# Optimization experiments

Hardware: AMD Instinct MI355X
Metric: run time of the kernel (lower is better)

The kernel has to match this reference:

```python
import jax, jax.numpy as jnp
import numpy as np

B, S, D, H = 4, 1024, 1024, 16
HD = D // H
EPS = 1e-5


def _layernorm(x, g, b):
    m = jnp.mean(x, axis=-1, keepdims=True)
    v = jnp.mean((x - m) ** 2, axis=-1, keepdims=True)
    return (x - m) * jax.lax.rsqrt(v + EPS) * g + b


def setup_inputs() -> dict:
    key = jax.random.key(0)
    ks = jax.random.split(key, 8)
    sc = 1.0 / np.sqrt(D)
    return {
        "x": jax.random.normal(ks[0], (B, S, D), dtype=jnp.float32),
        "seq_len": jax.random.randint(ks[1], (B,), 1, S + 1, dtype=jnp.int32),
        "Wq": jax.random.normal(ks[2], (D, D), dtype=jnp.float32) * sc,
        "bq": jnp.zeros((D,), dtype=jnp.float32),
        "Wk": jax.random.normal(ks[3], (D, D), dtype=jnp.float32) * sc,
        "bk": jnp.zeros((D,), dtype=jnp.float32),
        "Wv": jax.random.normal(ks[4], (D, D), dtype=jnp.float32) * sc,
        "bv": jnp.zeros((D,), dtype=jnp.float32),
        "ln_g": jnp.ones((HD,), dtype=jnp.float32),
        "ln_b": jnp.zeros((HD,), dtype=jnp.float32),
    }


def reference(x, seq_len, Wq, bq, Wk, bk, Wv, bv, ln_g, ln_b):
    # Faithful quirk: k and v are projections of the ALREADY projected q.
    q = x @ Wq.T + bq                      # [B,S,D]
    k = q @ Wk.T + bk
    v = q @ Wv.T + bv
    # [B,S,D] -> [B,H,S,HD]
    def split_heads(t):
        return t.reshape(B, S, H, HD).transpose(0, 2, 1, 3)
    q, k, v = split_heads(q), split_heads(k), split_heads(v)
    # shared per-head LayerNorm over head_dim
    q = _layernorm(q, ln_g, ln_b)
    k = _layernorm(k, ln_g, ln_b)
    v = _layernorm(v, ln_g, ln_b)
    # raw scores (no temperature scaling in the original; temperature=1.0 unused)
    scores = jnp.einsum("bhqd,bhkd->bhqk", q, k)
    # encoder_mask: multiplicative validity mask on key positions, repeated per head
    mask = (jnp.arange(S)[None, :] < seq_len[:, None]).astype(scores.dtype)  # [B,S]
    scores = scores * mask[:, None, None, :]
    attn = jax.nn.softmax(scores, axis=-1)
    # dropout is identity at inference
    out = jnp.einsum("bhqk,bhkd->bhqd", attn, v)
    return out.transpose(0, 2, 1, 3).reshape(B, S, D)
```

## Files before the change

### kernel.cpp

```cpp
#include <hip/hip_runtime.h>

#define B_  4
#define S_  1024
#define D_  1024
#define H_  16
#define HD_ 64
#define EPS_ 1e-5f

typedef _Float16 f16x8 __attribute__((ext_vector_type(8)));
typedef _Float16 f16x4 __attribute__((ext_vector_type(4)));
typedef __bf16 bf16x8 __attribute__((ext_vector_type(8)));
typedef float  f32x4  __attribute__((ext_vector_type(4)));
typedef unsigned short ushort8v __attribute__((ext_vector_type(8)));

static __device__ __forceinline__ unsigned short f2bf(float f) {
  union { float f; unsigned u; } v; v.f = f;
  unsigned r = v.u + 0x7fffu + ((v.u >> 16) & 1u);
  return (unsigned short)(r >> 16);
}
static __device__ __forceinline__ float bf2f(unsigned short u) {
  union { unsigned u; float f; } v; v.u = ((unsigned)u) << 16;
  return v.f;
}

#define GLD16(gp, lp) __builtin_amdgcn_global_load_lds( \
    (const __attribute__((address_space(1))) void*)(gp), \
    (__attribute__((address_space(3))) void*)(lp), 16, 0, 0)

__global__ __launch_bounds__(256) void cvt_all(
    const float* __restrict__ x,  _Float16* __restrict__ xh,
    const float* __restrict__ Wq, _Float16* __restrict__ wqh,
    const float* __restrict__ Wk, _Float16* __restrict__ wkh,
    const float* __restrict__ Wv, _Float16* __restrict__ wvh,
    float* __restrict__ Vtail) {
  int bid = blockIdx.x;
  if (bid >= 7168) {
    int i = (bid - 7168) * 1024 + threadIdx.x * 4;
    *(float4*)(Vtail + i) = make_float4(0.f, 0.f, 0.f, 0.f);
    return;
  }
  const float* src; _Float16* dst; int base;
  if (bid < 4096)      { src = x;  dst = xh;  base = bid; }
  else if (bid < 5120) { src = Wq; dst = wqh; base = bid - 4096; }
  else if (bid < 6144) { src = Wk; dst = wkh; base = bid - 5120; }
  else                 { src = Wv; dst = wvh; base = bid - 6144; }
  int i = base * 1024 + threadIdx.x * 4;
  float4 f = *(const float4*)(src + i);
  f16x4 h;
  h.x = (_Float16)f.x; h.y = (_Float16)f.y; h.z = (_Float16)f.z; h.w = (_Float16)f.w;
  *(f16x4*)(dst + i) = h;
}

__global__ __launch_bounds__(256, 2) void gemm_bt_bias(
    const _Float16* __restrict__ A,
    const _Float16* __restrict__ B0, const float* __restrict__ bias0,
    _Float16* __restrict__ C0,
    const _Float16* __restrict__ B1, const float* __restrict__ bias1,
    _Float16* __restrict__ C1,
    int M, int N, int K)
{
  const _Float16* Bm = blockIdx.z ? B1 : B0;
  const float* bias  = blockIdx.z ? bias1 : bias0;
  _Float16* C        = blockIdx.z ? C1 : C0;

  __shared__ _Float16 As[2 * 128 * 32];
  __shared__ _Float16 Bs[2 * 64 * 32];

  int tid  = threadIdx.x;
  int lane = tid & 63;
  int wave = tid >> 6;
  int wm = wave >> 1, wn = wave & 1;
  int qd = lane >> 4, l15 = lane & 15;

  long row0 = (long)blockIdx.y * 128;
  long col0 = (long)blockIdx.x * 64;

  int r_a = tid >> 2;
  int c_a = (tid & 3) * 8;

  f32x4 acc[4][2] = {};

  for (int kk = 0; kk < K; kk += 64) {
    GLD16(A  + (row0 + r_a) * K + kk + c_a,           As + tid * 8);
    GLD16(A  + (row0 + 64 + r_a) * K + kk + c_a,      As + 2048 + tid * 8);
    GLD16(A  + (row0 + r_a) * K + kk + 32 + c_a,      As + 4096 + tid * 8);
    GLD16(A  + (row0 + 64 + r_a) * K + kk + 32 + c_a, As + 6144 + tid * 8);
    GLD16(Bm + (col0 + r_a) * K + kk + c_a,           Bs + tid * 8);
    GLD16(Bm + (col0 + r_a) * K + kk + 32 + c_a,      Bs + 2048 + tid * 8);
    __syncthreads();

    for (int ks = 0; ks < 2; ks++) {
      f16x8 af[4], bfr[2];
      for (int t = 0; t < 4; t++)
        af[t]  = *(const f16x8*)(As + ks * 4096 + (wm * 64 + t * 16 + l15) * 32 + qd * 8);
      for (int j = 0; j < 2; j++)
        bfr[j] = *(const f16x8*)(Bs + ks * 2048 + (wn * 32 + j * 16 + l15) * 32 + qd * 8);
      for (int i = 0; i < 4; i++)
        for (int j = 0; j < 2; j++)
          acc[i][j] = __builtin_amdgcn_mfma_f32_16x16x32_f16(af[i], bfr[j], acc[i][j], 0, 0, 0);
    }
    __syncthreads();
  }

  for (int i = 0; i < 4; i++) {
    long row = row0 + wm * 64 + i * 16 + qd * 4;
    for (int j = 0; j < 2; j++) {
      long col = col0 + wn * 32 + j * 16 + l15;
      float bv = bias[col];
      for (int r = 0; r < 4; r++)
        C[(row + r) * N + col] = (_Float16)(acc[i][j][r] + bv);
    }
  }
}

__global__ __launch_bounds__(256, 2) void gemm_bt_bias128(
    const _Float16* __restrict__ A,
    const _Float16* __restrict__ B0, const float* __restrict__ bias0,
    _Float16* __restrict__ C0,
    const _Float16* __restrict__ B1, const float* __restrict__ bias1,
    _Float16* __restrict__ C1,
    int M, int N, int K)
{
  const _Float16* Bm = blockIdx.z ? B1 : B0;
  const float* bias  = blockIdx.z ? bias1 : bias0;
  _Float16* C        = blockIdx.z ? C1 : C0;

  __shared__ _Float16 As[2 * 128 * 32];
  __shared__ _Float16 Bs[2 * 128 * 32];

  int tid  = threadIdx.x;
  int lane = tid & 63;
  int wave = tid >> 6;
  int wm = wave >> 1, wn = wave & 1;
  int qd = lane >> 4, l15 = lane & 15;

  long row0 = (long)blockIdx.y * 128;
  long col0 = (long)blockIdx.x * 128;

  int r_a = tid >> 2;
  int c_a = (tid & 3) * 8;

  f32x4 acc[4][4] = {};

  for (int kk = 0; kk < K; kk += 64) {
    GLD16(A  + (row0 + r_a) * K + kk + c_a,           As + tid * 8);
    GLD16(A  + (row0 + 64 + r_a) * K + kk + c_a,      As + 2048 + tid * 8);
    GLD16(A  + (row0 + r_a) * K + kk + 32 + c_a,      As + 4096 + tid * 8);
    GLD16(A  + (row0 + 64 + r_a) * K + kk + 32 + c_a, As + 6144 + tid * 8);
    GLD16(Bm + (col0 + r_a) * K + kk + c_a,           Bs + tid * 8);
    GLD16(Bm + (col0 + 64 + r_a) * K + kk + c_a,      Bs + 2048 + tid * 8);
    GLD16(Bm + (col0 + r_a) * K + kk + 32 + c_a,      Bs + 4096 + tid * 8);
    GLD16(Bm + (col0 + 64 + r_a) * K + kk + 32 + c_a, Bs + 6144 + tid * 8);
    __syncthreads();

    for (int ks = 0; ks < 2; ks++) {
      f16x8 af[4], bfr[4];
      for (int t = 0; t < 4; t++) {
        af[t]  = *(const f16x8*)(As + ks * 4096 + (wm * 64 + t * 16 + l15) * 32 + qd * 8);
        bfr[t] = *(const f16x8*)(Bs + ks * 4096 + (wn * 64 + t * 16 + l15) * 32 + qd * 8);
      }
      for (int i = 0; i < 4; i++)
        for (int j = 0; j < 4; j++)
          acc[i][j] = __builtin_amdgcn_mfma_f32_16x16x32_f16(af[i], bfr[j], acc[i][j], 0, 0, 0);
    }
    __syncthreads();
  }

  for (int i = 0; i < 4; i++) {
    long row = row0 + wm * 64 + i * 16 + qd * 4;
    for (int j = 0; j < 4; j++) {
      long col = col0 + wn * 64 + j * 16 + l15;
      float bv = bias[col];
      for (int r = 0; r < 4; r++)
        C[(row + r) * N + col] = (_Float16)(acc[i][j][r] + bv);
    }
  }
}

__global__ __launch_bounds__(256) void ln_qkv(
    const _Float16* __restrict__ qh,
    const _Float16* __restrict__ kh,
    const _Float16* __restrict__ vh,
    const float* __restrict__ ln_g, const float* __restrict__ ln_b,
    const int* __restrict__ seq_len,
    _Float16* __restrict__ Qn,
    _Float16* __restrict__ Kn,
    unsigned short* __restrict__ Vt,
    float* __restrict__ Vtail)
{
  __shared__ unsigned short Vls[256][68];
  int tid = threadIdx.x;
  int s0 = blockIdx.x * 256;
  int h = blockIdx.y, b = blockIdx.z;
  long bh = (long)b * H_ + h;
  long s = s0 + tid;
  long inbase  = ((long)b * S_ + s) * D_ + (long)h * HD_;
  long outbase = (bh * S_ + s) * HD_;

  f16x8 rq[8], rk[8], rv[8];
  for (int i = 0; i < 8; i++) {
    rq[i] = *(const f16x8*)(qh + inbase + i * 8);
    rk[i] = *(const f16x8*)(kh + inbase + i * 8);
    rv[i] = *(const f16x8*)(vh + inbase + i * 8);
  }

  {
    float sum = 0.f, sq = 0.f;
    for (int i = 0; i < 8; i++)
      for (int j = 0; j < 8; j++) { float xv = (float)rq[i][j]; sum += xv; sq = fmaf(xv, xv, sq); }
    float m = sum * (1.f / 64.f);
    float inv = rsqrtf(sq * (1.f / 64.f) - m * m + EPS_);
    for (int i = 0; i < 8; i++) {
      f16x8 o;
      for (int j = 0; j < 8; j++)
        o[j] = (_Float16)(((float)rq[i][j] - m) * inv * ln_g[i * 8 + j] + ln_b[i * 8 + j]);
      *(f16x8*)(Qn + outbase + i * 8) = o;
    }
  }
  {
    float sum = 0.f, sq = 0.f;
    for (int i = 0; i < 8; i++)
      for (int j = 0; j < 8; j++) { float xv = (float)rk[i][j]; sum += xv; sq = fmaf(xv, xv, sq); }
    float m = sum * (1.f / 64.f);
    float inv = rsqrtf(sq * (1.f / 64.f) - m * m + EPS_);
    for (int i = 0; i < 8; i++) {
      f16x8 o;
      for (int j = 0; j < 8; j++)
        o[j] = (_Float16)(((float)rk[i][j] - m) * inv * ln_g[i * 8 + j] + ln_b[i * 8 + j]);
      *(f16x8*)(Kn + outbase + i * 8) = o;
    }
  }
  {
    float sum = 0.f, sq = 0.f;
    for (int i = 0; i < 8; i++)
      for (int j = 0; j < 8; j++) { float xv = (float)rv[i][j]; sum += xv; sq = fmaf(xv, xv, sq); }
    float m = sum * (1.f / 64.f);
    float inv = rsqrtf(sq * (1.f / 64.f) - m * m + EPS_);
    for (int i = 0; i < 8; i++)
      for (int j = 0; j < 8; j++)
        Vls[tid][i * 8 + j] = f2bf(((float)rv[i][j] - m) * inv * ln_g[i * 8 + j] + ln_b[i * 8 + j]);
  }
  __syncthreads();
  int d = tid >> 2, sc = tid & 3;
  int len = seq_len[b];
  long vbase = (bh * HD_ + d) * S_ + s0 + sc * 64;
  float tsum = 0.f;
  for (int j0 = 0; j0 < 64; j0 += 8) {
    ushort8v w;
    for (int jj = 0; jj < 8; jj++) {
      unsigned short ub = Vls[sc * 64 + j0 + jj][d];
      w[jj] = ub;
      if (s0 + sc * 64 + j0 + jj >= len) tsum += bf2f(ub);
    }
    *(ushort8v*)(Vt + vbase + j0) = w;
  }
  if (s0 + sc * 64 + 64 > len)
    atomicAdd(&Vtail[bh * HD_ + d], tsum);
}

__global__ __launch_bounds__(256, 4) void attn(
    const _Float16* __restrict__ Qn,
    const _Float16* __restrict__ Kn,
    const unsigned short* __restrict__ Vt,
    const float* __restrict__ Vtail,
    const int* __restrict__ seq_len,
    float* __restrict__ out)
{
  __shared__ _Float16 Ks[2][64 * 32];
  __shared__ unsigned short Vts[2][64 * 32];
  __shared__ __bf16 Ps[4][16 * 72];

  int tid = threadIdx.x, lane = tid & 63, wave = tid >> 6;
  int qd = lane >> 4, l15 = lane & 15;
  int b = blockIdx.x;
  int h = blockIdx.y;
  int q0 = blockIdx.z * 64;
  long bh = (long)b * H_ + h;
  int len = seq_len[b];
  int ntile = (len + 63) >> 6;

  int skey = tid >> 2;
  int schunk = (tid & 3) * 8;

  f16x8 qf[2];
  {
    const _Float16* qp = Qn + (bh * S_ + q0 + wave * 16 + l15) * HD_;
    qf[0] = *(const f16x8*)(qp + qd * 8);
    qf[1] = *(const f16x8*)(qp + 32 + qd * 8);
  }
  float tv[4];
  for (int t = 0; t < 4; t++) tv[t] = Vtail[bh * HD_ + t * 16 + l15];

  f32x4 o[4] = {};
  float den[4] = {0.f, 0.f, 0.f, 0.f};

  for (int kt = 0; kt < ntile; kt++) {
    GLD16(Kn + (bh * S_ + kt * 64 + skey) * HD_ + schunk,      &Ks[0][0] + tid * 8);
    GLD16(Kn + (bh * S_ + kt * 64 + skey) * HD_ + 32 + schunk, &Ks[1][0] + tid * 8);
    GLD16(Vt + (bh * HD_ + skey) * S_ + kt * 64 + schunk,      &Vts[0][0] + tid * 8);
    GLD16(Vt + (bh * HD_ + skey) * S_ + kt * 64 + 32 + schunk, &Vts[1][0] + tid * 8);
    __syncthreads();

    f32x4 sacc[4] = {};
    for (int tn = 0; tn < 4; tn++) {
      f16x8 kf0 = *(const f16x8*)(&Ks[0][0] + (tn * 16 + l15) * 32 + qd * 8);
      f16x8 kf1 = *(const f16x8*)(&Ks[1][0] + (tn * 16 + l15) * 32 + qd * 8);
      sacc[tn] = __builtin_amdgcn_mfma_f32_16x16x32_f16(qf[0], kf0, sacc[tn], 0, 0, 0);
      sacc[tn] = __builtin_amdgcn_mfma_f32_16x16x32_f16(qf[1], kf1, sacc[tn], 0, 0, 0);
    }

    if (kt * 64 + 64 <= len) {
      for (int tn = 0; tn < 4; tn++)
        for (int r = 0; r < 4; r++) {
          float p = __expf(sacc[tn][r]);
          __bf16 pb = (__bf16)p;
          den[r] += (float)pb;
          Ps[wave][(qd * 4 + r) * 72 + tn * 16 + l15] = pb;
        }
    } else {
      for (int tn = 0; tn < 4; tn++) {
        int kg = kt * 64 + tn * 16 + l15;
        bool valid = kg < len;
        for (int r = 0; r < 4; r++) {
          float p = valid ? __expf(sacc[tn][r]) : 0.f;
          __bf16 pb = (__bf16)p;
          den[r] += (float)pb;
          Ps[wave][(qd * 4 + r) * 72 + tn * 16 + l15] = pb;
        }
      }
    }

    bf16x8 pf0 = *(const bf16x8*)(&Ps[wave][l15 * 72 + qd * 8]);
    bf16x8 pf1 = *(const bf16x8*)(&Ps[wave][l15 * 72 + 32 + qd * 8]);
    for (int t = 0; t < 4; t++) {
      bf16x8 vf0 = *(const bf16x8*)(&Vts[0][0] + (t * 16 + l15) * 32 + qd * 8);
      bf16x8 vf1 = *(const bf16x8*)(&Vts[1][0] + (t * 16 + l15) * 32 + qd * 8);
      o[t] = __builtin_amdgcn_mfma_f32_16x16x32_bf16(pf0, vf0, o[t], 0, 0, 0);
      o[t] = __builtin_amdgcn_mfma_f32_16x16x32_bf16(pf1, vf1, o[t], 0, 0, 0);
    }
    __syncthreads();
  }

  for (int t = 0; t < 4; t++)
    for (int r = 0; r < 4; r++) o[t][r] += tv[t];

  float tden = (float)(S_ - len);
  for (int r = 0; r < 4; r++) {
    for (int off = 1; off < 16; off <<= 1)
      den[r] += __shfl_xor(den[r], off, 64);
    den[r] += tden;
  }

  for (int t = 0; t < 4; t++)
    for (int r = 0; r < 4; r++) {
      long s = q0 + wave * 16 + qd * 4 + r;
      long dcol = (long)h * HD_ + t * 16 + l15;
      out[((long)b * S_ + s) * D_ + dcol] = o[t][r] / den[r];
    }
}

extern "C" void kernel_launch(void* const* d_in, const int* in_sizes, int n_in,
                              void* d_out, int out_size, void* d_ws, size_t ws_size,
                              hipStream_t stream) {
  const float* x     = (const float*)d_in[0];
  const int*  seq    = (const int*)d_in[1];
  const float* Wq    = (const float*)d_in[2];
  const float* bq    = (const float*)d_in[3];
  const float* Wk    = (const float*)d_in[4];
  const float* bk    = (const float*)d_in[5];
  const float* Wv    = (const float*)d_in[6];
  const float* bv    = (const float*)d_in[7];
  const float* ln_g  = (const float*)d_in[8];
  const float* ln_b  = (const float*)d_in[9];
  float* out = (float*)d_out;

  char* ws = (char*)d_ws;
  _Float16* xh  = (_Float16*)(ws);
  _Float16* wqh = (_Float16*)(ws + (8l  << 20));
  _Float16* wkh = (_Float16*)(ws + (10l << 20));
  _Float16* wvh = (_Float16*)(ws + (12l << 20));
  float*    Vtail = (float*)(ws + (14l << 20));
  _Float16* qh  = (_Float16*)(ws + (16l << 20));
  _Float16* kh  = (_Float16*)(ws + (24l << 20));
  _Float16* vh  = (_Float16*)(ws + (32l << 20));
  _Float16* Qn  = (_Float16*)(ws + (40l << 20));
  _Float16* Kn  = (_Float16*)(ws + (48l << 20));
  unsigned short* Vt = (unsigned short*)(ws + (56l << 20));

  cvt_all<<<7172, 256, 0, stream>>>(x, xh, Wq, wqh, Wk, wkh, Wv, wvh, Vtail);

  dim3 g1(D_ / 64, (B_ * S_) / 128, 1);
  gemm_bt_bias<<<g1, 256, 0, stream>>>(xh, wqh, bq, qh, wqh, bq, qh,
                                       B_ * S_, D_, D_);
  dim3 g2(D_ / 128, (B_ * S_) / 128, 2);
  gemm_bt_bias128<<<g2, 256, 0, stream>>>(qh, wkh, bk, kh, wvh, bv, vh,
                                          B_ * S_, D_, D_);

  dim3 g3(S_ / 256, H_, B_);
  ln_qkv<<<g3, 256, 0, stream>>>(qh, kh, vh, ln_g, ln_b, seq, Qn, Kn, Vt, Vtail);

  dim3 g4(B_, H_, S_ / 64);
  attn<<<g4, 256, 0, stream>>>(Qn, Kn, Vt, Vtail, seq, out);
}
```

Measured before the change: 183.1 us.

## Fuse per-head LayerNorm and V transpose into projection GEMM epilogues

The per-head LayerNorm, the V transpose to bf16 and the masked-tail V sum move into the epilogues of the Q and K/V projection GEMMs, and the separate ln_qkv kernel goes away. Tile-to-warp mappings are rearranged so each wave owns full 64-wide head columns, and row statistics are reduced with lane shuffles. This removes one launch and the round trip of kh/vh through global memory. In exchange the epilogues use scattered narrow stores (per-lane f16 writes and 4-element Vt writes) instead of vectorized ones, and the Q GEMM writes both qh and Qn.

```diff
diff --git a/kernel.cpp b/kernel.cpp
--- a/kernel.cpp
+++ b/kernel.cpp
@@ -11,17 +11,8 @@
 typedef _Float16 f16x4 __attribute__((ext_vector_type(4)));
 typedef __bf16 bf16x8 __attribute__((ext_vector_type(8)));
 typedef float  f32x4  __attribute__((ext_vector_type(4)));
+typedef unsigned short ushort4v __attribute__((ext_vector_type(4)));
 typedef unsigned short ushort8v __attribute__((ext_vector_type(8)));
-
-static __device__ __forceinline__ unsigned short f2bf(float f) {
-  union { float f; unsigned u; } v; v.f = f;
-  unsigned r = v.u + 0x7fffu + ((v.u >> 16) & 1u);
-  return (unsigned short)(r >> 16);
-}
-static __device__ __forceinline__ float bf2f(unsigned short u) {
-  union { unsigned u; float f; } v; v.u = ((unsigned)u) << 16;
-  return v.f;
-}
 
 #define GLD16(gp, lp) __builtin_amdgcn_global_load_lds( \
     (const __attribute__((address_space(1))) void*)(gp), \
@@ -51,20 +42,105 @@
   *(f16x4*)(dst + i) = h;
 }
 
-__global__ __launch_bounds__(256, 2) void gemm_bt_bias(
+__global__ __launch_bounds__(256, 2) void gemm_q_ln(
     const _Float16* __restrict__ A,
-    const _Float16* __restrict__ B0, const float* __restrict__ bias0,
-    _Float16* __restrict__ C0,
-    const _Float16* __restrict__ B1, const float* __restrict__ bias1,
-    _Float16* __restrict__ C1,
-    int M, int N, int K)
+    const _Float16* __restrict__ Bw,
+    const float* __restrict__ bias,
+    const float* __restrict__ ln_g, const float* __restrict__ ln_b,
+    _Float16* __restrict__ qh,
+    _Float16* __restrict__ Qn)
 {
-  const _Float16* Bm = blockIdx.z ? B1 : B0;
-  const float* bias  = blockIdx.z ? bias1 : bias0;
-  _Float16* C        = blockIdx.z ? C1 : C0;
-
   __shared__ _Float16 As[2 * 128 * 32];
   __shared__ _Float16 Bs[2 * 64 * 32];
+
+  int tid  = threadIdx.x;
+  int lane = tid & 63;
+  int wave = tid >> 6;
+  int qd = lane >> 4, l15 = lane & 15;
+
+  long row0 = (long)blockIdx.y * 128;
+  long col0 = (long)blockIdx.x * 64;
+
+  int r_a = tid >> 2;
+  int c_a = (tid & 3) * 8;
+
+  f32x4 acc[2][4] = {};
+
+  for (int kk = 0; kk < D_; kk += 64) {
+    GLD16(A  + (row0 + r_a) * D_ + kk + c_a,           As + tid * 8);
+    GLD16(A  + (row0 + 64 + r_a) * D_ + kk + c_a,      As + 2048 + tid * 8);
+    GLD16(A  + (row0 + r_a) * D_ + kk + 32 + c_a,      As + 4096 + tid * 8);
+    GLD16(A  + (row0 + 64 + r_a) * D_ + kk + 32 + c_a, As + 6144 + tid * 8);
+    GLD16(Bw + (col0 + r_a) * D_ + kk + c_a,           Bs + tid * 8);
+    GLD16(Bw + (col0 + r_a) * D_ + kk + 32 + c_a,      Bs + 2048 + tid * 8);
+    __syncthreads();
+
+    for (int ks = 0; ks < 2; ks++) {
+      f16x8 af[2], bfr[4];
+      for (int i = 0; i < 2; i++)
+        af[i]  = *(const f16x8*)(As + ks * 4096 + (wave * 32 + i * 16 + l15) * 32 + qd * 8);
+      for (int j = 0; j < 4; j++)
+        bfr[j] = *(const f16x8*)(Bs + ks * 2048 + (j * 16 + l15) * 32 + qd * 8);
+      for (int i = 0; i < 2; i++)
+        for (int j = 0; j < 4; j++)
+          acc[i][j] = __builtin_amdgcn_mfma_f32_16x16x32_f16(af[i], bfr[j], acc[i][j], 0, 0, 0);
+    }
+    __syncthreads();
+  }
+
+  int h = blockIdx.x;
+  long rw = row0 + wave * 32;
+  int bb = (int)(rw >> 10);
+  long bh = (long)bb * H_ + h;
+  float gv[4], bl[4], bc[4];
+  for (int j = 0; j < 4; j++) {
+    int d = j * 16 + l15;
+    gv[j] = ln_g[d]; bl[j] = ln_b[d]; bc[j] = bias[h * 64 + d];
+  }
+  for (int i = 0; i < 2; i++) {
+    float m4[4], i4[4];
+    for (int r = 0; r < 4; r++) {
+      float s = 0.f, q = 0.f;
+      for (int j = 0; j < 4; j++) {
+        float y = acc[i][j][r] + bc[j];
+        s += y; q = fmaf(y, y, q);
+      }
+      for (int off = 1; off < 16; off <<= 1) {
+        s += __shfl_xor(s, off, 64);
+        q += __shfl_xor(q, off, 64);
+      }
+      float m = s * (1.f / 64.f);
+      m4[r] = m;
+      i4[r] = rsqrtf(q * (1.f / 64.f) - m * m + EPS_);
+    }
+    for (int r = 0; r < 4; r++) {
+      long srow = rw + i * 16 + qd * 4 + r;
+      long sloc = srow & (S_ - 1);
+      for (int j = 0; j < 4; j++) {
+        float y = acc[i][j][r] + bc[j];
+        qh[srow * D_ + h * 64 + j * 16 + l15] = (_Float16)y;
+        Qn[(bh * S_ + sloc) * HD_ + j * 16 + l15] =
+            (_Float16)((y - m4[r]) * i4[r] * gv[j] + bl[j]);
+      }
+    }
+  }
+}
+
+__global__ __launch_bounds__(256, 2) void gemm_kv_ln(
+    const _Float16* __restrict__ A,
+    const _Float16* __restrict__ Bk, const float* __restrict__ bk,
+    const _Float16* __restrict__ Bv, const float* __restrict__ bv,
+    const float* __restrict__ ln_g, const float* __restrict__ ln_b,
+    const int* __restrict__ seq_len,
+    _Float16* __restrict__ Kn,
+    unsigned short* __restrict__ Vt,
+    float* __restrict__ Vtail)
+{
+  const _Float16* Bm = blockIdx.z ? Bv : Bk;
+  const float* bias  = blockIdx.z ? bv : bk;
+
+  __shared__ _Float16 As[2 * 128 * 32];
+  __shared__ _Float16 Bs[2 * 128 * 32];
 
   int tid  = threadIdx.x;
   int lane = tid & 63;
@@ -73,84 +149,22 @@
   int qd = lane >> 4, l15 = lane & 15;
 
   long row0 = (long)blockIdx.y * 128;
-  long col0 = (long)blockIdx.x * 64;
+  long col0 = (long)blockIdx.x * 128;
 
   int r_a = tid >> 2;
   int c_a = (tid & 3) * 8;
 
-  f32x4 acc[4][2] = {};
-
-  for (int kk = 0; kk < K; kk += 64) {
-    GLD16(A  + (row0 + r_a) * K + kk + c_a,           As + tid * 8);
-    GLD16(A  + (row0 + 64 + r_a) * K + kk + c_a,      As + 2048 + tid * 8);
-    GLD16(A  + (row0 + r_a) * K + kk + 32 + c_a,      As + 4096 + tid * 8);
-    GLD16(A  + (row0 + 64 + r_a) * K + kk + 32 + c_a, As + 6144 + tid * 8);
-    GLD16(Bm + (col0 + r_a) * K + kk + c_a,           Bs + tid * 8);
-    GLD16(Bm + (col0 + r_a) * K + kk + 32 + c_a,      Bs + 2048 + tid * 8);
-    __syncthreads();
-
-    for (int ks = 0; ks < 2; ks++) {
-      f16x8 af[4], bfr[2];
-      for (int t = 0; t < 4; t++)
-        af[t]  = *(const f16x8*)(As + ks * 4096 + (wm * 64 + t * 16 + l15) * 32 + qd * 8);
-      for (int j = 0; j < 2; j++)
-        bfr[j] = *(const f16x8*)(Bs + ks * 2048 + (wn * 32 + j * 16 + l15) * 32 + qd * 8);
-      for (int i = 0; i < 4; i++)
-        for (int j = 0; j < 2; j++)
-          acc[i][j] = __builtin_amdgcn_mfma_f32_16x16x32_f16(af[i], bfr[j], acc[i][j], 0, 0, 0);
-    }
-    __syncthreads();
-  }
-
-  for (int i = 0; i < 4; i++) {
-    long row = row0 + wm * 64 + i * 16 + qd * 4;
-    for (int j = 0; j < 2; j++) {
-      long col = col0 + wn * 32 + j * 16 + l15;
-      float bv = bias[col];
-      for (int r = 0; r < 4; r++)
-        C[(row + r) * N + col] = (_Float16)(acc[i][j][r] + bv);
-    }
-  }
-}
-
-__global__ __launch_bounds__(256, 2) void gemm_bt_bias128(
-    const _Float16* __restrict__ A,
-    const _Float16* __restrict__ B0, const float* __restrict__ bias0,
-    _Float16* __restrict__ C0,
-    const _Float16* __restrict__ B1, const float* __restrict__ bias1,
-    _Float16* __restrict__ C1,
-    int M, int N, int K)
-{
-  const _Float16* Bm = blockIdx.z ? B1 : B0;
-  const float* bias  = blockIdx.z ? bias1 : bias0;
-  _Float16* C        = blockIdx.z ? C1 : C0;
-
-  __shared__ _Float16 As[2 * 128 * 32];
-  __shared__ _Float16 Bs[2 * 128 * 32];
-
-  int tid  = threadIdx.x;
-  int lane = tid & 63;
-  int wave = tid >> 6;
-  int wm = wave >> 1, wn = wave & 1;
-  int qd = lane >> 4, l15 = lane & 15;
-
-  long row0 = (long)blockIdx.y * 128;
-  long col0 = (long)blockIdx.x * 128;
-
-  int r_a = tid >> 2;
-  int c_a = (tid & 3) * 8;
-
   f32x4 acc[4][4] = {};
 
-  for (int kk = 0; kk < K; kk += 64) {
-    GLD16(A  + (row0 + r_a) * K + kk + c_a,           As + tid * 8);
-    GLD16(A  + (row0 + 64 + r_a) * K + kk + c_a,      As + 2048 + tid * 8);
-    GLD16(A  + (row0 + r_a) * K + kk + 32 + c_a,      As + 4096 + tid * 8);
-    GLD16(A  + (row0 + 64 + r_a) * K + kk + 32 + c_a, As + 6144 + tid * 8);
-    GLD16(Bm + (col0 + r_a) * K + kk + c_a,           Bs + tid * 8);
-    GLD16(Bm + (col0 + 64 + r_a) * K + kk + c_a,      Bs + 2048 + tid * 8);
-    GLD16(Bm + (col0 + r_a) * K + kk + 32 + c_a,      Bs + 4096 + tid * 8);
-    GLD16(Bm + (col0 + 64 + r_a) * K + kk + 32 + c_a, Bs + 6144 + tid * 8);
+  for (int kk = 0; kk < D_; kk += 64) {
+    GLD16(A  + (row0 + r_a) * D_ + kk + c_a,           As + tid * 8);
+    GLD16(A  + (row0 + 64 + r_a) * D_ + kk + c_a,      As + 2048 + tid * 8);
+    GLD16(A  + (row0 + r_a) * D_ + kk + 32 + c_a,      As + 4096 + tid * 8);
+    GLD16(A  + (row0 + 64 + r_a) * D_ + kk + 32 + c_a, As + 6144 + tid * 8);
+    GLD16(Bm + (col0 + r_a) * D_ + kk + c_a,           Bs + tid * 8);
+    GLD16(Bm + (col0 + 64 + r_a) * D_ + kk + c_a,      Bs + 2048 + tid * 8);
+    GLD16(Bm + (col0 + r_a) * D_ + kk + 32 + c_a,      Bs + 4096 + tid * 8);
+    GLD16(Bm + (col0 + 64 + r_a) * D_ + kk + 32 + c_a, Bs + 6144 + tid * 8);
     __syncthreads();
 
     for (int ks = 0; ks < 2; ks++) {
@@ -166,96 +180,79 @@
     __syncthreads();
   }
 
-  for (int i = 0; i < 4; i++) {
-    long row = row0 + wm * 64 + i * 16 + qd * 4;
-    for (int j = 0; j < 4; j++) {
-      long col = col0 + wn * 64 + j * 16 + l15;
-      float bv = bias[col];
-      for (int r = 0; r < 4; r++)
-        C[(row + r) * N + col] = (_Float16)(acc[i][j][r] + bv);
-    }
-  }
-}
-
-__global__ __launch_bounds__(256) void ln_qkv(
-    const _Float16* __restrict__ qh,
-    const _Float16* __restrict__ kh,
-    const _Float16* __restrict__ vh,
-    const float* __restrict__ ln_g, const float* __restrict__ ln_b,
-    const int* __restrict__ seq_len,
-    _Float16* __restrict__ Qn,
-    _Float16* __restrict__ Kn,
-    unsigned short* __restrict__ Vt,
-    float* __restrict__ Vtail)
-{
-  __shared__ unsigned short Vls[256][68];
-  int tid = threadIdx.x;
-  int s0 = blockIdx.x * 256;
-  int h = blockIdx.y, b = blockIdx.z;
-  long bh = (long)b * H_ + h;
-  long s = s0 + tid;
-  long inbase  = ((long)b * S_ + s) * D_ + (long)h * HD_;
-  long outbase = (bh * S_ + s) * HD_;
-
-  f16x8 rq[8], rk[8], rv[8];
-  for (int i = 0; i < 8; i++) {
-    rq[i] = *(const f16x8*)(qh + inbase + i * 8);
-    rk[i] = *(const f16x8*)(kh + inbase + i * 8);
-    rv[i] = *(const f16x8*)(vh + inbase + i * 8);
-  }
-
-  {
-    float sum = 0.f, sq = 0.f;
-    for (int i = 0; i < 8; i++)
-      for (int j = 0; j < 8; j++) { float xv = (float)rq[i][j]; sum += xv; sq = fmaf(xv, xv, sq); }
-    float m = sum * (1.f / 64.f);
-    float inv = rsqrtf(sq * (1.f / 64.f) - m * m + EPS_);
-    for (int i = 0; i < 8; i++) {
-      f16x8 o;
-      for (int j = 0; j < 8; j++)
-        o[j] = (_Float16)(((float)rq[i][j] - m) * inv * ln_g[i * 8 + j] + ln_b[i * 8 + j]);
-      *(f16x8*)(Qn + outbase + i * 8) = o;
-    }
-  }
-  {
-    float sum = 0.f, sq = 0.f;
-    for (int i = 0; i < 8; i++)
-      for (int j = 0; j < 8; j++) { float xv = (float)rk[i][j]; sum += xv; sq = fmaf(xv, xv, sq); }
-    float m = sum * (1.f / 64.f);
-    float inv = rsqrtf(sq * (1.f / 64.f) - m * m + EPS_);
-    for (int i = 0; i < 8; i++) {
-      f16x8 o;
-      for (int j = 0; j < 8; j++)
-        o[j] = (_Float16)(((float)rk[i][j] - m) * inv * ln_g[i * 8 + j] + ln_b[i * 8 + j]);
-      *(f16x8*)(Kn + outbase + i * 8) = o;
-    }
-  }
-  {
-    float sum = 0.f, sq = 0.f;
-    for (int i = 0; i < 8; i++)
-      for (int j = 0; j < 8; j++) { float xv = (float)rv[i][j]; sum += xv; sq = fmaf(xv, xv, sq); }
-    float m = sum * (1.f / 64.f);
-    float inv = rsqrtf(sq * (1.f / 64.f) - m * m + EPS_);
-    for (int i = 0; i < 8; i++)
-      for (int j = 0; j < 8; j++)
-        Vls[tid][i * 8 + j] = f2bf(((float)rv[i][j] - m) * inv * ln_g[i * 8 + j] + ln_b[i * 8 + j]);
-  }
-  __syncthreads();
-  int d = tid >> 2, sc = tid & 3;
-  int len = seq_len[b];
-  long vbase = (bh * HD_ + d) * S_ + s0 + sc * 64;
-  float tsum = 0.f;
-  for (int j0 = 0; j0 < 64; j0 += 8) {
-    ushort8v w;
-    for (int jj = 0; jj < 8; jj++) {
-      unsigned short ub = Vls[sc * 64 + j0 + jj][d];
-      w[jj] = ub;
-      if (s0 + sc * 64 + j0 + jj >= len) tsum += bf2f(ub);
-    }
-    *(ushort8v*)(Vt + vbase + j0) = w;
-  }
-  if (s0 + sc * 64 + 64 > len)
-    atomicAdd(&Vtail[bh * HD_ + d], tsum);
+  int h = blockIdx.x * 2 + wn;
+  long rw = row0 + wm * 64;
+  int bb = (int)(rw >> 10);
+  long bh = (long)bb * H_ + h;
+  float gv[4], bl[4], bc[4];
+  for (int j = 0; j < 4; j++) {
+    int d = j * 16 + l15;
+    gv[j] = ln_g[d]; bl[j] = ln_b[d]; bc[j] = bias[h * 64 + d];
+  }
+
+  if (blockIdx.z == 0) {
+    for (int i = 0; i < 4; i++) {
+      float m4[4], i4[4];
+      for (int r = 0; r < 4; r++) {
+        float s = 0.f, q = 0.f;
+        for (int j = 0; j < 4; j++) {
+          float y = acc[i][j][r] + bc[j];
+          s += y; q = fmaf(y, y, q);
+        }
+        for (int off = 1; off < 16; off <<= 1) {
+          s += __shfl_xor(s, off, 64);
+          q += __shfl_xor(q, off, 64);
+        }
+        float m = s * (1.f / 64.f);
+        m4[r] = m;
+        i4[r] = rsqrtf(q * (1.f / 64.f) - m * m + EPS_);
+      }
+      for (int r = 0; r < 4; r++) {
+        long sloc = (rw + i * 16 + qd * 4 + r) & (S_ - 1);
+        for (int j = 0; j < 4; j++) {
+          float y = acc[i][j][r] + bc[j];
+          Kn[(bh * S_ + sloc) * HD_ + j * 16 + l15] =
+              (_Float16)((y - m4[r]) * i4[r] * gv[j] + bl[j]);
+        }
+      }
+    }
+  } else {
+    int len = seq_len[bb];
+    float tsum[4] = {0.f, 0.f, 0.f, 0.f};
+    for (int i = 0; i < 4; i++) {
+      float m4[4], i4[4];
+      for (int r = 0; r < 4; r++) {
+        float s = 0.f, q = 0.f;
+        for (int j = 0; j < 4; j++) {
+          float y = acc[i][j][r] + bc[j];
+          s += y; q = fmaf(y, y, q);
+        }
+        for (int off = 1; off < 16; off <<= 1) {
+          s += __shfl_xor(s, off, 64);
+          q += __shfl_xor(q, off, 64);
+        }
+        float m = s * (1.f / 64.f);
+        m4[r] = m;
+        i4[r] = rsqrtf(q * (1.f / 64.f) - m * m + EPS_);
+      }
+      int s0loc = (int)((rw + i * 16 + qd * 4) & (S_ - 1));
+      for (int j = 0; j < 4; j++) {
+        ushort4v w;
+        for (int r = 0; r < 4; r++) {
+          float y = acc[i][j][r] + bc[j];
+          float vo = (y - m4[r]) * i4[r] * gv[j] + bl[j];
+          __bf16 vb = (__bf16)vo;
+          union { __bf16 hh; unsigned short uu; } cv; cv.hh = vb;
+          w[r] = cv.uu;
+          if (s0loc + r >= len) tsum[j] += (float)vb;
+        }
+        *(ushort4v*)(Vt + (bh * HD_ + j * 16 + l15) * S_ + s0loc) = w;
+      }
+    }
+    if (((int)(rw & (S_ - 1)) + 64) > len)
+      for (int j = 0; j < 4; j++)
+        atomicAdd(&Vtail[bh * HD_ + j * 16 + l15], tsum[j]);
+  }
 }
 
 __global__ __launch_bounds__(256, 4) void attn(
@@ -381,23 +378,18 @@
   _Float16* wvh = (_Float16*)(ws + (12l << 20));
   float*    Vtail = (float*)(ws + (14l << 20));
   _Float16* qh  = (_Float16*)(ws + (16l << 20));
-  _Float16* kh  = (_Float16*)(ws + (24l << 20));
-  _Float16* vh  = (_Float16*)(ws + (32l << 20));
   _Float16* Qn  = (_Float16*)(ws + (40l << 20));
   _Float16* Kn  = (_Float16*)(ws + (48l << 20));
   unsigned short* Vt = (unsigned short*)(ws + (56l << 20));
 
   cvt_all<<<7172, 256, 0, stream>>>(x, xh, Wq, wqh, Wk, wkh, Wv, wvh, Vtail);
 
-  dim3 g1(D_ / 64, (B_ * S_) / 128, 1);
-  gemm_bt_bias<<<g1, 256, 0, stream>>>(xh, wqh, bq, qh, wqh, bq, qh,
-                                       B_ * S_, D_, D_);
+  dim3 g1(D_ / 64, (B_ * S_) / 128);
+  gemm_q_ln<<<g1, 256, 0, stream>>>(xh, wqh, bq, ln_g, ln_b, qh, Qn);
+
   dim3 g2(D_ / 128, (B_ * S_) / 128, 2);
-  gemm_bt_bias128<<<g2, 256, 0, stream>>>(qh, wkh, bk, kh, wvh, bv, vh,
-                                          B_ * S_, D_, D_);
-
-  dim3 g3(S_ / 256, H_, B_);
-  ln_qkv<<<g3, 256, 0, stream>>>(qh, kh, vh, ln_g, ln_b, seq, Qn, Kn, Vt, Vtail);
+  gemm_kv_ln<<<g2, 256, 0, stream>>>(qh, wkh, bk, wvh, bv, ln_g, ln_b, seq,
+                                     Kn, Vt, Vtail);
 
   dim3 g4(B_, H_, S_ / 64);
   attn<<<g4, 256, 0, stream>>>(Qn, Kn, Vt, Vtail, seq, out);
```

New measurement: 168.6 us. 1.09x faster.
